# Optimization experiments

Measured on AMD Instinct MI355X. Metric: run time of the kernel, lower is better.

Reference implementation:

```python
import jax, jax.numpy as jnp
import numpy as np

V, E, H, C, T = 50000, 512, 1024, 1221, 4096


def setup_inputs() -> dict:
    key = jax.random.key(0)
    ks = jax.random.split(key, 8)
    s = 1.0 / np.sqrt(H)  # PyTorch LSTM/Linear init scale
    return {
        "x": jax.random.randint(ks[0], (T,), 0, V),
        "emb_table": jax.random.normal(ks[1], (V, E), jnp.float32),
        "W_ih": jax.random.uniform(ks[2], (4 * H, 2 * E), jnp.float32, -s, s),
        "W_hh": jax.random.uniform(ks[3], (4 * H, H), jnp.float32, -s, s),
        "b_ih": jax.random.uniform(ks[4], (4 * H,), jnp.float32, -s, s),
        "b_hh": jax.random.uniform(ks[5], (4 * H,), jnp.float32, -s, s),
        "W_out": jax.random.uniform(ks[6], (C, H), jnp.float32, -s, s),
        "b_out": jax.random.uniform(ks[7], (C,), jnp.float32, -s, s),
    }


def reference(x, emb_table, W_ih, W_hh, b_ih, b_hh, W_out, b_out):
    emb = emb_table[x]                       # [T, E]
    last = emb[-1]                           # [E] embedding of final token
    n = emb.shape[0] - 1
    # each step input: concat(word_i, word_last) -> [T-1, 2E]
    xs = jnp.concatenate(
        [emb[:-1], jnp.broadcast_to(last, (n, last.shape[0]))], axis=1
    )
    # Precompute input projections for all steps in one GEMM: [T-1, 4H]
    x_gates = xs @ W_ih.T + b_ih + b_hh
    hdim = W_hh.shape[1]

    def step(carry, xg):
        h, c = carry
        gates = xg + h @ W_hh.T              # [4H], PyTorch gate order i,f,g,o
        i, f, g, o = jnp.split(gates, 4)
        i = jax.nn.sigmoid(i)
        f = jax.nn.sigmoid(f)
        g = jnp.tanh(g)
        o = jax.nn.sigmoid(o)
        c = f * c + i * g
        h = o * jnp.tanh(c)
        return (h, c), h

    h0 = jnp.zeros((hdim,), dtype=x_gates.dtype)
    c0 = jnp.zeros((hdim,), dtype=x_gates.dtype)
    _, hs = jax.lax.scan(step, (h0, c0), x_gates)  # hs: [T-1, H]
    out = hs @ W_out.T + b_out                     # [T-1, C]
    return out[None, :, :]                         # (1, T-1, C)
```

## Files before the change

### kernel.cpp

```cpp
#include <hip/hip_runtime.h>
#include <math.h>

#define NSTEP 4095
#define EDIM  512
#define HDIM  1024
#define GDIM  4096
#define KDIM  1024
#define CDIM  1221
#define SNWG  64
#define UNITS 16

__device__ __forceinline__ float sigmoidf_(float v) {
    return 1.0f / (1.0f + __expf(-v));
}
__device__ __forceinline__ float tanhf_(float v) {
    v = fminf(fmaxf(v, -15.0f), 15.0f);
    const float e2 = __expf(2.0f * v);
    return (e2 - 1.0f) / (e2 + 1.0f);
}

__global__ __launch_bounds__(256) void gemm_emb_kernel(
    const int* __restrict__ x, const float* __restrict__ emb,
    const float* __restrict__ W, const float* __restrict__ b_ih,
    const float* __restrict__ b_hh, float* __restrict__ xg)
{
    __shared__ float As[8][128];
    __shared__ float Bs[8][128];
    const int tid = threadIdx.x;
    const int bm = blockIdx.y * 128, bn = blockIdx.x * 128;
    const int tx = tid & 15, ty = tid >> 4;
    const int lrow = tid >> 1;
    const int lk4  = (tid & 1) * 4;
    const int lastTok = x[NSTEP];
    const int am = bm + lrow;
    const int tokRow = (am < NSTEP) ? x[am] : 0;
    const int bnrow = bn + lrow;

    float acc[8][8];
#pragma unroll
    for (int i = 0; i < 8; ++i)
#pragma unroll
        for (int j = 0; j < 8; ++j) acc[i][j] = 0.0f;

    for (int k0 = 0; k0 < KDIM; k0 += 8) {
        const int k = k0 + lk4;
        float4 av = make_float4(0.f, 0.f, 0.f, 0.f);
        if (am < NSTEP) {
            const int tok = (k < EDIM) ? tokRow : lastTok;
            const int kk  = (k < EDIM) ? k : (k - EDIM);
            av = *(const float4*)(emb + (size_t)tok * EDIM + kk);
        }
        const float4 bv = *(const float4*)(W + (size_t)bnrow * KDIM + k);
        __syncthreads();
        As[lk4 + 0][lrow] = av.x; As[lk4 + 1][lrow] = av.y;
        As[lk4 + 2][lrow] = av.z; As[lk4 + 3][lrow] = av.w;
        Bs[lk4 + 0][lrow] = bv.x; Bs[lk4 + 1][lrow] = bv.y;
        Bs[lk4 + 2][lrow] = bv.z; Bs[lk4 + 3][lrow] = bv.w;
        __syncthreads();
#pragma unroll
        for (int kk = 0; kk < 8; ++kk) {
            const float4 a0 = *(const float4*)&As[kk][ty * 4];
            const float4 a1 = *(const float4*)&As[kk][ty * 4 + 64];
            const float4 b0 = *(const float4*)&Bs[kk][tx * 4];
            const float4 b1 = *(const float4*)&Bs[kk][tx * 4 + 64];
            const float a[8] = {a0.x, a0.y, a0.z, a0.w, a1.x, a1.y, a1.z, a1.w};
            const float b[8] = {b0.x, b0.y, b0.z, b0.w, b1.x, b1.y, b1.z, b1.w};
#pragma unroll
            for (int i = 0; i < 8; ++i)
#pragma unroll
                for (int j = 0; j < 8; ++j) acc[i][j] += a[i] * b[j];
        }
    }
#pragma unroll
    for (int i = 0; i < 8; ++i) {
        const int m = bm + ((i < 4) ? (ty * 4 + i) : (64 + ty * 4 + i - 4));
        if (m >= NSTEP) continue;
#pragma unroll
        for (int j = 0; j < 8; ++j) {
            const int n = bn + ((j < 4) ? (tx * 4 + j) : (64 + tx * 4 + j - 4));
            xg[(size_t)m * GDIM + n] = acc[i][j] + b_ih[n] + b_hh[n];
        }
    }
}

__global__ __launch_bounds__(256) void gemm_out_kernel(
    const float* __restrict__ A, const float* __restrict__ W,
    const float* __restrict__ bias, float* __restrict__ C)
{
    __shared__ float As[8][128];
    __shared__ float Bs[8][128];
    const int tid = threadIdx.x;
    const int bm = blockIdx.y * 128, bn = blockIdx.x * 128;
    const int tx = tid & 15, ty = tid >> 4;
    const int lrow = tid >> 1;
    const int lk4  = (tid & 1) * 4;
    const int am = bm + lrow;
    const int bnrow = bn + lrow;

    float acc[8][8];
#pragma unroll
    for (int i = 0; i < 8; ++i)
#pragma unroll
        for (int j = 0; j < 8; ++j) acc[i][j] = 0.0f;

    for (int k0 = 0; k0 < KDIM; k0 += 8) {
        const int k = k0 + lk4;
        float4 av = make_float4(0.f, 0.f, 0.f, 0.f);
        if (am < NSTEP) av = *(const float4*)(A + (size_t)am * KDIM + k);
        float4 bv = make_float4(0.f, 0.f, 0.f, 0.f);
        if (bnrow < CDIM) bv = *(const float4*)(W + (size_t)bnrow * KDIM + k);
        __syncthreads();
        As[lk4 + 0][lrow] = av.x; As[lk4 + 1][lrow] = av.y;
        As[lk4 + 2][lrow] = av.z; As[lk4 + 3][lrow] = av.w;
        Bs[lk4 + 0][lrow] = bv.x; Bs[lk4 + 1][lrow] = bv.y;
        Bs[lk4 + 2][lrow] = bv.z; Bs[lk4 + 3][lrow] = bv.w;
        __syncthreads();
#pragma unroll
        for (int kk = 0; kk < 8; ++kk) {
            const float4 a0 = *(const float4*)&As[kk][ty * 4];
            const float4 a1 = *(const float4*)&As[kk][ty * 4 + 64];
            const float4 b0 = *(const float4*)&Bs[kk][tx * 4];
            const float4 b1 = *(const float4*)&Bs[kk][tx * 4 + 64];
            const float a[8] = {a0.x, a0.y, a0.z, a0.w, a1.x, a1.y, a1.z, a1.w};
            const float b[8] = {b0.x, b0.y, b0.z, b0.w, b1.x, b1.y, b1.z, b1.w};
#pragma unroll
            for (int i = 0; i < 8; ++i)
#pragma unroll
                for (int j = 0; j < 8; ++j) acc[i][j] += a[i] * b[j];
        }
    }
#pragma unroll
    for (int i = 0; i < 8; ++i) {
        const int m = bm + ((i < 4) ? (ty * 4 + i) : (64 + ty * 4 + i - 4));
        if (m >= NSTEP) continue;
#pragma unroll
        for (int j = 0; j < 8; ++j) {
            const int n = bn + ((j < 4) ? (tx * 4 + j) : (64 + tx * 4 + j - 4));
            if (n < CDIM) C[(size_t)m * CDIM + n] = acc[i][j] + bias[n];
        }
    }
}

__global__ __launch_bounds__(1024, 4) void scan_kernel(
    const float* __restrict__ xg, const float* __restrict__ Whh,
    float* __restrict__ hs, unsigned long long* hb)
{
    __shared__ float h_s[HDIM];
    __shared__ float gate_s[64];
    __shared__ float c_s[UNITS];
    const int g = blockIdx.x, tid = threadIdx.x;
    const int lane = tid & 63, wv = tid >> 6;
    const int seg = tid & 15, lr = tid >> 4;
    const int q = lr >> 4, j = lr & 15;
    const int grow = q * HDIM + g * UNITS + j;

    float4 w4[16];
#pragma unroll
    for (int i = 0; i < 16; ++i)
        w4[i] = *(const float4*)(Whh + (size_t)grow * KDIM + i * 64 + seg * 4);
#pragma unroll
    for (int i = 0; i < 16; ++i)
        asm volatile("" : "+v"(w4[i].x), "+v"(w4[i].y), "+v"(w4[i].z), "+v"(w4[i].w));

    for (int i = tid; i < HDIM; i += 1024) h_s[i] = 0.0f;
    if (tid < UNITS) c_s[tid] = 0.0f;
    __syncthreads();

    for (int t = 1; t <= NSTEP; ++t) {
        float xgv = 0.0f;
        if (seg == 0) xgv = xg[(size_t)(t - 1) * GDIM + grow];

        if (t > 1) {
            const int par = (t - 1) & 1;
            const int el = wv * 64 + lane;
            const int want = t - 1;
            unsigned long long v;
            for (;;) {
                v = __hip_atomic_load(&hb[par * HDIM + el], __ATOMIC_RELAXED,
                                      __HIP_MEMORY_SCOPE_AGENT);
                if ((int)(v >> 32) == want) break;
            }
            h_s[el] = __uint_as_float((unsigned)v);
        }
        __syncthreads();

        float acc = 0.0f;
#pragma unroll
        for (int i = 0; i < 16; ++i) {
            const float4 h4 = *(const float4*)&h_s[i * 64 + seg * 4];
            acc += w4[i].x * h4.x + w4[i].y * h4.y +
                   w4[i].z * h4.z + w4[i].w * h4.w;
        }
        acc += __shfl_xor(acc, 1, 64);
        acc += __shfl_xor(acc, 2, 64);
        acc += __shfl_xor(acc, 4, 64);
        acc += __shfl_xor(acc, 8, 64);
        if (seg == 0) gate_s[lr] = acc + xgv;
        __syncthreads();

        if (tid < UNITS) {
            const int jj = tid;
            const float ig = sigmoidf_(gate_s[jj]);
            const float fg = sigmoidf_(gate_s[16 + jj]);
            const float gg = tanhf_(gate_s[32 + jj]);
            const float og = sigmoidf_(gate_s[48 + jj]);
            const float c  = fg * c_s[jj] + ig * gg;
            c_s[jj] = c;
            const float h = og * tanhf_(c);
            hs[(size_t)(t - 1) * HDIM + g * UNITS + jj] = h;
            const unsigned long long pv =
                ((unsigned long long)(unsigned)t << 32) | __float_as_uint(h);
            __hip_atomic_store(&hb[(t & 1) * HDIM + g * UNITS + jj], pv,
                               __ATOMIC_RELAXED, __HIP_MEMORY_SCOPE_AGENT);
        }
    }
}

extern "C" void kernel_launch(void* const* d_in, const int* in_sizes, int n_in,
                              void* d_out, int out_size, void* d_ws, size_t ws_size,
                              hipStream_t stream)
{
    const int*   x     = (const int*)d_in[0];
    const float* emb   = (const float*)d_in[1];
    const float* W_ih  = (const float*)d_in[2];
    const float* W_hh  = (const float*)d_in[3];
    const float* b_ih  = (const float*)d_in[4];
    const float* b_hh  = (const float*)d_in[5];
    const float* W_out = (const float*)d_in[6];
    const float* b_out = (const float*)d_in[7];
    float* out = (float*)d_out;

    float* xg = (float*)d_ws;
    float* hs = xg + (size_t)NSTEP * GDIM;
    unsigned long long* hb =
        (unsigned long long*)(hs + (size_t)NSTEP * HDIM);

    dim3 blk(256);
    dim3 g1(GDIM / 128, 32);
    gemm_emb_kernel<<<g1, blk, 0, stream>>>(x, emb, W_ih, b_ih, b_hh, xg);

    scan_kernel<<<dim3(SNWG), dim3(1024), 0, stream>>>(xg, W_hh, hs, hb);

    dim3 g2((CDIM + 127) / 128, 32);
    gemm_out_kernel<<<g2, blk, 0, stream>>>(hs, W_out, b_out, out);
}
```

Baseline: 8.281 ms.

## Spread LSTM scan over 256 workgroups with one hidden unit per wavefront

The persistent recurrent kernel now launches 256 workgroups of 256 threads instead of 64 of 1024. Each wavefront owns one hidden unit and computes its four gates, with the gate values moved by shuffles and the cell state held in a register. This removes the second block barrier and the shared gate/cell arrays. Each thread now polls four hidden-state flags per step in one batched loop, and h_s is double-buffered. The cost is more workgroups spinning on the global flags and more polling traffic per step, and 256 co-resident workgroups are required for the spin-wait not to deadlock.

```diff
diff --git a/kernel.cpp b/kernel.cpp
--- a/kernel.cpp
+++ b/kernel.cpp
@@ -7,8 +7,8 @@
 #define GDIM  4096
 #define KDIM  1024
 #define CDIM  1221
-#define SNWG  64
-#define UNITS 16
+#define SNWG  256
+#define SNT   256
 
 __device__ __forceinline__ float sigmoidf_(float v) {
     return 1.0f / (1.0f + __expf(-v));
@@ -141,76 +141,88 @@
     }
 }
 
-__global__ __launch_bounds__(1024, 4) void scan_kernel(
+__global__ __launch_bounds__(256) void scan_kernel(
     const float* __restrict__ xg, const float* __restrict__ Whh,
     float* __restrict__ hs, unsigned long long* hb)
 {
-    __shared__ float h_s[HDIM];
-    __shared__ float gate_s[64];
-    __shared__ float c_s[UNITS];
-    const int g = blockIdx.x, tid = threadIdx.x;
-    const int lane = tid & 63, wv = tid >> 6;
-    const int seg = tid & 15, lr = tid >> 4;
-    const int q = lr >> 4, j = lr & 15;
-    const int grow = q * HDIM + g * UNITS + j;
+    __shared__ float h_s[2][HDIM];
+    const int tid  = threadIdx.x;
+    const int wv   = tid >> 6;
+    const int lane = tid & 63;
+    const int q    = lane >> 4;
+    const int seg  = lane & 15;
+    const int unit = blockIdx.x * 4 + wv;
+    const int grow = q * HDIM + unit;
 
     float4 w4[16];
 #pragma unroll
-    for (int i = 0; i < 16; ++i)
-        w4[i] = *(const float4*)(Whh + (size_t)grow * KDIM + i * 64 + seg * 4);
-#pragma unroll
-    for (int i = 0; i < 16; ++i)
-        asm volatile("" : "+v"(w4[i].x), "+v"(w4[i].y), "+v"(w4[i].z), "+v"(w4[i].w));
-
-    for (int i = tid; i < HDIM; i += 1024) h_s[i] = 0.0f;
-    if (tid < UNITS) c_s[tid] = 0.0f;
+    for (int j = 0; j < 16; ++j)
+        w4[j] = *(const float4*)(Whh + (size_t)grow * KDIM + j * 64 + seg * 4);
+#pragma unroll
+    for (int j = 0; j < 16; ++j)
+        asm volatile("" : "+v"(w4[j].x), "+v"(w4[j].y), "+v"(w4[j].z), "+v"(w4[j].w));
+
+    for (int i = tid; i < HDIM; i += SNT) h_s[0][i] = 0.0f;
     __syncthreads();
 
+    float c = 0.0f;
+
     for (int t = 1; t <= NSTEP; ++t) {
+        const int par = (t - 1) & 1;
+
         float xgv = 0.0f;
         if (seg == 0) xgv = xg[(size_t)(t - 1) * GDIM + grow];
 
         if (t > 1) {
-            const int par = (t - 1) & 1;
-            const int el = wv * 64 + lane;
             const int want = t - 1;
-            unsigned long long v;
-            for (;;) {
-                v = __hip_atomic_load(&hb[par * HDIM + el], __ATOMIC_RELAXED,
-                                      __HIP_MEMORY_SCOPE_AGENT);
-                if ((int)(v >> 32) == want) break;
-            }
-            h_s[el] = __uint_as_float((unsigned)v);
-        }
-        __syncthreads();
-
-        float acc = 0.0f;
-#pragma unroll
-        for (int i = 0; i < 16; ++i) {
-            const float4 h4 = *(const float4*)&h_s[i * 64 + seg * 4];
-            acc += w4[i].x * h4.x + w4[i].y * h4.y +
-                   w4[i].z * h4.z + w4[i].w * h4.w;
+            const unsigned long long* p = hb + (size_t)par * HDIM + tid;
+            unsigned long long v0 = 0, v1 = 0, v2 = 0, v3 = 0;
+            unsigned pend = 0xFu;
+            do {
+                if (pend & 1u) v0 = __hip_atomic_load(p,       __ATOMIC_RELAXED, __HIP_MEMORY_SCOPE_AGENT);
+                if (pend & 2u) v1 = __hip_atomic_load(p + 256, __ATOMIC_RELAXED, __HIP_MEMORY_SCOPE_AGENT);
+                if (pend & 4u) v2 = __hip_atomic_load(p + 512, __ATOMIC_RELAXED, __HIP_MEMORY_SCOPE_AGENT);
+                if (pend & 8u) v3 = __hip_atomic_load(p + 768, __ATOMIC_RELAXED, __HIP_MEMORY_SCOPE_AGENT);
+                if ((pend & 1u) && (int)(v0 >> 32) == want) pend &= ~1u;
+                if ((pend & 2u) && (int)(v1 >> 32) == want) pend &= ~2u;
+                if ((pend & 4u) && (int)(v2 >> 32) == want) pend &= ~4u;
+                if ((pend & 8u) && (int)(v3 >> 32) == want) pend &= ~8u;
+            } while (pend);
+            h_s[par][tid      ] = __uint_as_float((unsigned)v0);
+            h_s[par][tid + 256] = __uint_as_float((unsigned)v1);
+            h_s[par][tid + 512] = __uint_as_float((unsigned)v2);
+            h_s[par][tid + 768] = __uint_as_float((unsigned)v3);
+        }
+        __syncthreads();
+
+        float acc = xgv;
+#pragma unroll
+        for (int j = 0; j < 16; ++j) {
+            const float4 h4 = *(const float4*)&h_s[par][j * 64 + seg * 4];
+            acc += w4[j].x * h4.x + w4[j].y * h4.y +
+                   w4[j].z * h4.z + w4[j].w * h4.w;
         }
         acc += __shfl_xor(acc, 1, 64);
         acc += __shfl_xor(acc, 2, 64);
         acc += __shfl_xor(acc, 4, 64);
         acc += __shfl_xor(acc, 8, 64);
-        if (seg == 0) gate_s[lr] = acc + xgv;
-        __syncthreads();
-
-        if (tid < UNITS) {
-            const int jj = tid;
-            const float ig = sigmoidf_(gate_s[jj]);
-            const float fg = sigmoidf_(gate_s[16 + jj]);
-            const float gg = tanhf_(gate_s[32 + jj]);
-            const float og = sigmoidf_(gate_s[48 + jj]);
-            const float c  = fg * c_s[jj] + ig * gg;
-            c_s[jj] = c;
-            const float h = og * tanhf_(c);
-            hs[(size_t)(t - 1) * HDIM + g * UNITS + jj] = h;
+        const float g0 = __shfl(acc,  0, 64);
+        const float g1 = __shfl(acc, 16, 64);
+        const float g2 = __shfl(acc, 32, 64);
+        const float g3 = __shfl(acc, 48, 64);
+
+        const float ig = sigmoidf_(g0);
+        const float fg = sigmoidf_(g1);
+        const float gg = tanhf_(g2);
+        const float og = sigmoidf_(g3);
+        c = fg * c + ig * gg;
+        const float h = og * tanhf_(c);
+
+        if (lane == 0) {
+            hs[(size_t)(t - 1) * HDIM + unit] = h;
             const unsigned long long pv =
                 ((unsigned long long)(unsigned)t << 32) | __float_as_uint(h);
-            __hip_atomic_store(&hb[(t & 1) * HDIM + g * UNITS + jj], pv,
+            __hip_atomic_store(&hb[(size_t)(t & 1) * HDIM + unit], pv,
                                __ATOMIC_RELAXED, __HIP_MEMORY_SCOPE_AGENT);
         }
     }
@@ -239,7 +251,7 @@
     dim3 g1(GDIM / 128, 32);
     gemm_emb_kernel<<<g1, blk, 0, stream>>>(x, emb, W_ih, b_ih, b_hh, xg);
 
-    scan_kernel<<<dim3(SNWG), dim3(1024), 0, stream>>>(xg, W_hh, hs, hb);
+    scan_kernel<<<dim3(SNWG), dim3(SNT), 0, stream>>>(xg, W_hh, hs, hb);
 
     dim3 g2((CDIM + 127) / 128, 32);
     gemm_out_kernel<<<g2, blk, 0, stream>>>(hs, W_out, b_out, out);
```

After: 15.67 ms. +89.2%, slower.
